# Kernel tuning notes

Hardware: AMD Instinct MI355X
Metric: run time of the kernel (lower is better)

The kernel has to match this reference:

```python
import jax, jax.numpy as jnp
import numpy as np

IN_CH, OUT_CH = 32, 32
MODES1, MODES2 = 16, 16
B, L, H, W = 8, 16, 64, 33


def setup_inputs() -> dict:
    key = jax.random.key(0)
    k = jax.random.split(key, 6)
    scale = 1.0 / (IN_CH * OUT_CH)
    wshape = (IN_CH, OUT_CH, MODES1, MODES2)
    return {
        "x_re": jax.random.normal(k[0], (B, L, IN_CH, H, W), dtype=jnp.float32),
        "x_im": jax.random.normal(k[1], (B, L, IN_CH, H, W), dtype=jnp.float32),
        "w1_re": scale * jax.random.normal(k[2], wshape, dtype=jnp.float32),
        "w1_im": scale * jax.random.normal(k[3], wshape, dtype=jnp.float32),
        "w2_re": scale * jax.random.normal(k[4], wshape, dtype=jnp.float32),
        "w2_im": scale * jax.random.normal(k[5], wshape, dtype=jnp.float32),
    }


def _mul2d(x, w):
    # x: [B, L, C_in, m1, m2] complex; w: [C_in, C_out, m1, m2] complex
    return jnp.einsum("blcij,coij->bloij", x, w)


def reference(x_re, x_im, w1_re, w1_im, w2_re, w2_im):
    x = jax.lax.complex(x_re, x_im)          # [B, L, C, H, W] complex64
    w1 = jax.lax.complex(w1_re, w1_im)       # [C_in, C_out, m1, m2]
    w2 = jax.lax.complex(w2_re, w2_im)
    Bx, Lx, Cx, Hx, Wx = x.shape
    m1 = min(Hx, MODES1)
    m2 = min(Wx, MODES2)

    out = jnp.zeros((Bx, Lx, OUT_CH, Hx, Wx), dtype=x.dtype)
    # low positive frequencies (top-left corner)
    out = out.at[:, :, :, :m1, :m2].set(
        _mul2d(x[:, :, :, :m1, :m2], w1[:, :, :m1, :m2]))
    # low negative frequencies along H (bottom-left corner)
    if Hx > 1 and (Hx > MODES1 or Wx > MODES2):
        out = out.at[:, :, :, -m1:, :m2].set(
            _mul2d(x[:, :, :, -m1:, :m2], w2[:, :, :m1, :m2]))
    # return complex result as trailing real/imag dim (float32)
    return jnp.stack([out.real, out.imag], axis=-1)
```

## Files before the change

kernel.cpp:

```cpp
#include <hip/hip_runtime.h>

#define HW 2112L
typedef float f32x4 __attribute__((ext_vector_type(4)));
typedef short s16x8 __attribute__((ext_vector_type(8)));

#define WT_PLANE 1048576L
#define OFF_WHR 0L
#define OFF_WLR (WT_PLANE)
#define OFF_WHI (2*WT_PLANE)
#define OFF_WLI (3*WT_PLANE)

__device__ __forceinline__ ushort f2bf(float f) {
    unsigned u = __float_as_uint(f);
    u += 0x7FFF + ((u >> 16) & 1);
    return (ushort)(u >> 16);
}
__device__ __forceinline__ void split_bf(float v, ushort& hi, ushort& lo) {
    hi = f2bf(v);
    float hf = __uint_as_float(((unsigned)hi) << 16);
    lo = f2bf(v - hf);
}

__global__ __launch_bounds__(256) void w_prep(
    const float* __restrict__ w1_re, const float* __restrict__ w1_im,
    const float* __restrict__ w2_re, const float* __restrict__ w2_im,
    char* __restrict__ ws)
{
    const int tid = threadIdx.x, bid = blockIdx.x;
    const int r = bid >> 5, i = (bid >> 1) & 15, nt = bid & 1;
    const float* wre = r ? w2_re : w1_re;
    const float* wim = r ? w2_im : w1_im;
    const int j = tid >> 4, col = tid & 15, o = nt * 16 + col;
    const int modeLin = (r * 16 + i) * 16 + j;
    s16x8* phr = (s16x8*)(ws + OFF_WHR);
    s16x8* plr = (s16x8*)(ws + OFF_WLR);
    s16x8* phi = (s16x8*)(ws + OFF_WHI);
    s16x8* pli = (s16x8*)(ws + OFF_WLI);
    #pragma unroll
    for (int kg = 0; kg < 4; ++kg) {
        s16x8 hr, lr, hi2, li2;
        #pragma unroll
        for (int e = 0; e < 8; ++e) {
            int c = kg * 8 + e;
            long src = ((long)(c * 32 + o) * 16 + i) * 16 + j;
            ushort a, b;
            split_bf(wre[src], a, b); hr[e] = (short)a; lr[e] = (short)b;
            split_bf(wim[src], a, b); hi2[e] = (short)a; li2[e] = (short)b;
        }
        long off = (long)(modeLin * 2 + nt) * 64 + kg * 16 + col;
        phr[off] = hr; plr[off] = lr; phi[off] = hi2; pli[off] = li2;
    }
}

__global__ __launch_bounds__(256) void spectral_main(
    const float* __restrict__ x_re, const float* __restrict__ x_im,
    float* __restrict__ out, const char* __restrict__ ws)
{
    const int tid = threadIdx.x, bid = blockIdx.x;

    if (bid & 1) {
        const int fid = bid >> 1;
        int gtid = fid * 256 + tid, n = 256 * 256;
        float4* out4 = (float4*)out;
        const float4 z = make_float4(0.f, 0.f, 0.f, 0.f);
        for (int idx = gtid; idx < 4096 * 528; idx += n) {
            int plane = idx / 528;
            int k = idx - plane * 528;
            out4[(long)plane * 1056 + 264 + k] = z;
        }
        return;
    }

    const int gid = bid >> 1;
    const int r = gid >> 7, i = (gid >> 3) & 15, bt = gid & 7;
    const int h = r ? 48 + i : i;
    const int bl0 = bt * 16;
    const int modeBase = (r * 16 + i) * 16;

    __shared__ __align__(16) char smem[69632];
    float2 (*xls)[16][17] = reinterpret_cast<float2(*)[16][17]>(smem);
    float2 (*stg)[17]     = reinterpret_cast<float2(*)[17]>(smem);

    for (int it = 0; it < 32; ++it) {
        int idx = it * 256 + tid;
        int j = idx & 15, rowid = idx >> 4;
        int c = rowid >> 4, bl = rowid & 15;
        long src = ((long)(bl0 + bl) * 32 + c) * HW + h * 33 + j;
        xls[c][bl][j] = make_float2(x_re[src], x_im[src]);
    }
    __syncthreads();

    const int wave = tid >> 6, lane = tid & 63;
    const int m = lane & 15, ks = lane >> 4;

    const s16x8* Bwhr = (const s16x8*)(ws + OFF_WHR);
    const s16x8* Bwlr = (const s16x8*)(ws + OFF_WLR);
    const s16x8* Bwhi = (const s16x8*)(ws + OFF_WHI);
    const s16x8* Bwli = (const s16x8*)(ws + OFF_WLI);

    float2 res[4][2][4];

    #pragma unroll
    for (int jj = 0; jj < 4; ++jj) {
        const int j = wave * 4 + jj;
        const int modeLin = modeBase + j;

        s16x8 Ahr, Alr, Ahi, Ali;
        #pragma unroll
        for (int e = 0; e < 8; ++e) {
            float2 v = xls[ks * 8 + e][m][j];
            ushort a, b;
            split_bf(v.x, a, b); Ahr[e] = (short)a; Alr[e] = (short)b;
            split_bf(v.y, a, b); Ahi[e] = (short)a; Ali[e] = (short)b;
        }

        #pragma unroll
        for (int nt = 0; nt < 2; ++nt) {
            long boff = (long)(modeLin * 2 + nt) * 64 + lane;
            s16x8 Bhr = Bwhr[boff], Blr = Bwlr[boff];
            s16x8 Bhi = Bwhi[boff], Bli = Bwli[boff];

            f32x4 accP = (f32x4)0.0f, accN = (f32x4)0.0f, accI = (f32x4)0.0f;
            accP = __builtin_amdgcn_mfma_f32_16x16x32_bf16(Ahr, Bhr, accP, 0, 0, 0);
            accP = __builtin_amdgcn_mfma_f32_16x16x32_bf16(Ahr, Blr, accP, 0, 0, 0);
            accP = __builtin_amdgcn_mfma_f32_16x16x32_bf16(Alr, Bhr, accP, 0, 0, 0);
            accN = __builtin_amdgcn_mfma_f32_16x16x32_bf16(Ahi, Bhi, accN, 0, 0, 0);
            accN = __builtin_amdgcn_mfma_f32_16x16x32_bf16(Ahi, Bli, accN, 0, 0, 0);
            accN = __builtin_amdgcn_mfma_f32_16x16x32_bf16(Ali, Bhi, accN, 0, 0, 0);
            accI = __builtin_amdgcn_mfma_f32_16x16x32_bf16(Ahr, Bhi, accI, 0, 0, 0);
            accI = __builtin_amdgcn_mfma_f32_16x16x32_bf16(Ahr, Bli, accI, 0, 0, 0);
            accI = __builtin_amdgcn_mfma_f32_16x16x32_bf16(Alr, Bhi, accI, 0, 0, 0);
            accI = __builtin_amdgcn_mfma_f32_16x16x32_bf16(Ahi, Bhr, accI, 0, 0, 0);
            accI = __builtin_amdgcn_mfma_f32_16x16x32_bf16(Ahi, Blr, accI, 0, 0, 0);
            accI = __builtin_amdgcn_mfma_f32_16x16x32_bf16(Ali, Bhr, accI, 0, 0, 0);

            #pragma unroll
            for (int q = 0; q < 4; ++q)
                res[jj][nt][q] = make_float2(accP[q] - accN[q], accI[q]);
        }
    }
    __syncthreads();

    const int rbase = (lane >> 4) * 4, colo = lane & 15;
    #pragma unroll
    for (int jj = 0; jj < 4; ++jj)
        #pragma unroll
        for (int nt = 0; nt < 2; ++nt)
            #pragma unroll
            for (int q = 0; q < 4; ++q)
                stg[(rbase + q) * 32 + nt * 16 + colo][wave * 4 + jj] = res[jj][nt][q];
    __syncthreads();

    float2* out2 = (float2*)out;
    #pragma unroll 2
    for (int t = 0; t < 66; ++t) {
        int idx = t * 256 + tid;
        int row = idx / 33;
        int k = idx - row * 33;
        int bl = row >> 5, o = row & 31;
        float2 v = (k < 16) ? stg[row][k] : make_float2(0.f, 0.f);
        long dst = (((long)(bl0 + bl) * 32 + o) * 64 + h) * 33 + k;
        out2[dst] = v;
    }
}

extern "C" void kernel_launch(void* const* d_in, const int* in_sizes, int n_in,
                              void* d_out, int out_size, void* d_ws, size_t ws_size,
                              hipStream_t stream) {
    const float* x_re  = (const float*)d_in[0];
    const float* x_im  = (const float*)d_in[1];
    const float* w1_re = (const float*)d_in[2];
    const float* w1_im = (const float*)d_in[3];
    const float* w2_re = (const float*)d_in[4];
    const float* w2_im = (const float*)d_in[5];
    float* out = (float*)d_out;
    char* ws = (char*)d_ws;

    w_prep<<<dim3(64), dim3(256), 0, stream>>>(w1_re, w1_im, w2_re, w2_im, ws);
    spectral_main<<<dim3(512), dim3(256), 0, stream>>>(x_re, x_im, out, ws);
}
```

Measured before the change: 39.99 us.

## Halve batch tile per compute block, split weight prep, rebalance compute/zero-fill roles

Compute blocks now handle 8 batch-time rows instead of 16, which halves shared memory and doubles the number of compute blocks to 512. A 2:1 compute-to-zero-fill role split gives 768 total blocks. w_prep is split across twice as many blocks, launch bounds request 3 blocks per SM, and the x load is restructured into 4-wide strided reads. The aim is more parallelism and occupancy. The cost is that half of each MFMA tile's M dimension is wasted, because rows 8-15 duplicate rows 0-7 via lane&7, so the same MFMA work now covers half the useful output.

```diff
diff --git a/kernel.cpp b/kernel.cpp
--- a/kernel.cpp
+++ b/kernel.cpp
@@ -27,7 +27,7 @@
     char* __restrict__ ws)
 {
     const int tid = threadIdx.x, bid = blockIdx.x;
-    const int r = bid >> 5, i = (bid >> 1) & 15, nt = bid & 1;
+    const int r = bid >> 6, i = (bid >> 2) & 15, nt = (bid >> 1) & 1, kh = bid & 1;
     const float* wre = r ? w2_re : w1_re;
     const float* wim = r ? w2_im : w1_im;
     const int j = tid >> 4, col = tid & 15, o = nt * 16 + col;
@@ -37,7 +37,8 @@
     s16x8* phi = (s16x8*)(ws + OFF_WHI);
     s16x8* pli = (s16x8*)(ws + OFF_WLI);
     #pragma unroll
-    for (int kg = 0; kg < 4; ++kg) {
+    for (int kk = 0; kk < 2; ++kk) {
+        const int kg = kh * 2 + kk;
         s16x8 hr, lr, hi2, li2;
         #pragma unroll
         for (int e = 0; e < 8; ++e) {
@@ -52,14 +53,15 @@
     }
 }
 
-__global__ __launch_bounds__(256) void spectral_main(
+__global__ __launch_bounds__(256, 3) void spectral_main(
     const float* __restrict__ x_re, const float* __restrict__ x_im,
     float* __restrict__ out, const char* __restrict__ ws)
 {
     const int tid = threadIdx.x, bid = blockIdx.x;
+    const int role = bid % 3;
 
-    if (bid & 1) {
-        const int fid = bid >> 1;
+    if (role == 2) {
+        const int fid = bid / 3;
         int gtid = fid * 256 + tid, n = 256 * 256;
         float4* out4 = (float4*)out;
         const float4 z = make_float4(0.f, 0.f, 0.f, 0.f);
@@ -71,27 +73,34 @@
         return;
     }
 
-    const int gid = bid >> 1;
-    const int r = gid >> 7, i = (gid >> 3) & 15, bt = gid & 7;
+    const int cid = (bid / 3) * 2 + role;
+    const int r = cid >> 8, i = (cid >> 4) & 15, bt = cid & 15;
     const int h = r ? 48 + i : i;
-    const int bl0 = bt * 16;
+    const int bl0 = bt * 8;
     const int modeBase = (r * 16 + i) * 16;
 
-    __shared__ __align__(16) char smem[69632];
-    float2 (*xls)[16][17] = reinterpret_cast<float2(*)[16][17]>(smem);
-    float2 (*stg)[17]     = reinterpret_cast<float2(*)[17]>(smem);
+    __shared__ __align__(16) char smem[34816];
+    float2 (*xls)[8][17] = reinterpret_cast<float2(*)[8][17]>(smem);
+    float2 (*stg)[17]    = reinterpret_cast<float2(*)[17]>(smem);
 
-    for (int it = 0; it < 32; ++it) {
-        int idx = it * 256 + tid;
-        int j = idx & 15, rowid = idx >> 4;
-        int c = rowid >> 4, bl = rowid & 15;
-        long src = ((long)(bl0 + bl) * 32 + c) * HW + h * 33 + j;
-        xls[c][bl][j] = make_float2(x_re[src], x_im[src]);
+    #pragma unroll
+    for (int p = 0; p < 4; ++p) {
+        int idx = p * 256 + tid;
+        int j4 = idx & 3, row = idx >> 2;
+        int c = row >> 3, bl = row & 7;
+        long base = ((long)((bl0 + bl) * 32 + c)) * HW + h * 33 + j4 * 4;
+        float r0 = x_re[base + 0], r1 = x_re[base + 1], r2 = x_re[base + 2], r3 = x_re[base + 3];
+        float i0 = x_im[base + 0], i1 = x_im[base + 1], i2 = x_im[base + 2], i3 = x_im[base + 3];
+        xls[c][bl][j4 * 4 + 0] = make_float2(r0, i0);
+        xls[c][bl][j4 * 4 + 1] = make_float2(r1, i1);
+        xls[c][bl][j4 * 4 + 2] = make_float2(r2, i2);
+        xls[c][bl][j4 * 4 + 3] = make_float2(r3, i3);
     }
     __syncthreads();
 
     const int wave = tid >> 6, lane = tid & 63;
-    const int m = lane & 15, ks = lane >> 4;
+    const int m = lane & 7;
+    const int ks = lane >> 4;
 
     const s16x8* Bwhr = (const s16x8*)(ws + OFF_WHR);
     const s16x8* Bwlr = (const s16x8*)(ws + OFF_WLR);
@@ -141,25 +150,26 @@
     }
     __syncthreads();
 
-    const int rbase = (lane >> 4) * 4, colo = lane & 15;
-    #pragma unroll
-    for (int jj = 0; jj < 4; ++jj)
+    if (ks < 2) {
+        const int rbase = ks * 4, colo = lane & 15;
         #pragma unroll
-        for (int nt = 0; nt < 2; ++nt)
+        for (int jj = 0; jj < 4; ++jj)
             #pragma unroll
-            for (int q = 0; q < 4; ++q)
-                stg[(rbase + q) * 32 + nt * 16 + colo][wave * 4 + jj] = res[jj][nt][q];
+            for (int nt = 0; nt < 2; ++nt)
+                #pragma unroll
+                for (int q = 0; q < 4; ++q)
+                    stg[(rbase + q) * 32 + nt * 16 + colo][wave * 4 + jj] = res[jj][nt][q];
+    }
     __syncthreads();
 
     float2* out2 = (float2*)out;
     #pragma unroll 2
-    for (int t = 0; t < 66; ++t) {
+    for (int t = 0; t < 33; ++t) {
         int idx = t * 256 + tid;
         int row = idx / 33;
         int k = idx - row * 33;
-        int bl = row >> 5, o = row & 31;
         float2 v = (k < 16) ? stg[row][k] : make_float2(0.f, 0.f);
-        long dst = (((long)(bl0 + bl) * 32 + o) * 64 + h) * 33 + k;
+        long dst = ((long)(bl0 * 32 + row) * 64 + h) * 33 + k;
         out2[dst] = v;
     }
 }
@@ -176,6 +186,6 @@
     float* out = (float*)d_out;
     char* ws = (char*)d_ws;
 
-    w_prep<<<dim3(64), dim3(256), 0, stream>>>(w1_re, w1_im, w2_re, w2_im, ws);
-    spectral_main<<<dim3(512), dim3(256), 0, stream>>>(x_re, x_im, out, ws);
+    w_prep<<<dim3(128), dim3(256), 0, stream>>>(w1_re, w1_im, w2_re, w2_im, ws);
+    spectral_main<<<dim3(768), dim3(256), 0, stream>>>(x_re, x_im, out, ws);
 }
```

After: 34.68 us. -13.3%, faster.
